# Kernel optimization log

Hardware: AMD Instinct MI355X
Metric: run time of the kernel (lower is better)

The kernel has to match this reference:

```python
import jax, jax.numpy as jnp
import numpy as np

B, S, L, T = 32, 512, 20, 16
E, H, D = 300, 128, 128
V = 50000
SEG = S // T


def _gru_dir(x, Wi, Wh, bi, bh, reverse):
    """One direction of torch-style GRU. x: (B,S,E). Returns (outs (B,S,H), h_final (B,H))."""
    xs = jnp.swapaxes(x, 0, 1)  # (S,B,E)
    h0 = jnp.zeros((x.shape[0], H), x.dtype)

    def step(h, x_t):
        gi = x_t @ Wi.T + bi          # (B,3H) gates order: r,z,n (torch)
        gh = h @ Wh.T + bh
        r = jax.nn.sigmoid(gi[:, :H] + gh[:, :H])
        z = jax.nn.sigmoid(gi[:, H:2 * H] + gh[:, H:2 * H])
        n = jnp.tanh(gi[:, 2 * H:] + r * gh[:, 2 * H:])
        h_new = (1.0 - z) * n + z * h
        return h_new, h_new

    hN, hs = jax.lax.scan(step, h0, xs, reverse=reverse)
    return jnp.swapaxes(hs, 0, 1), hN


def setup_inputs() -> dict:
    key = jax.random.key(0)
    ks = jax.random.split(key, 16)
    word_ids = jax.random.randint(ks[0], (B, S, L), 0, V, dtype=jnp.int32)
    # contiguous, full-coverage topic segments, 1-based boundaries (as in the torch code)
    starts = jnp.tile(jnp.arange(T, dtype=jnp.int32) * SEG + 1, (B, 1))
    ends = jnp.tile((jnp.arange(T, dtype=jnp.int32) + 1) * SEG, (B, 1))
    sent2topic = jnp.tile((jnp.arange(S, dtype=jnp.int32) // SEG), (B, 1))
    sc = 0.08
    return {
        "word_ids": word_ids, "starts": starts, "ends": ends, "sent2topic": sent2topic,
        "embed_table": jax.random.normal(ks[1], (V, E), jnp.float32) * 0.6,
        "Wi_f": jax.random.normal(ks[2], (3 * H, E), jnp.float32) * sc,
        "Wh_f": jax.random.normal(ks[3], (3 * H, H), jnp.float32) * sc,
        "bi_f": jax.random.normal(ks[4], (3 * H,), jnp.float32) * sc,
        "bh_f": jax.random.normal(ks[5], (3 * H,), jnp.float32) * sc,
        "Wi_b": jax.random.normal(ks[6], (3 * H, E), jnp.float32) * sc,
        "Wh_b": jax.random.normal(ks[7], (3 * H, H), jnp.float32) * sc,
        "bi_b": jax.random.normal(ks[8], (3 * H,), jnp.float32) * sc,
        "bh_b": jax.random.normal(ks[9], (3 * H,), jnp.float32) * sc,
        "W_att": jax.random.normal(ks[10], (4 * H, 4 * H), jnp.float32) * 0.05,
        "v_att": jax.random.normal(ks[11], (4 * H, 1), jnp.float32) * 0.05,
        "W1": jax.random.normal(ks[12], (D, 4 * H), jnp.float32) * 0.05,
        "b1": jax.random.normal(ks[13], (D,), jnp.float32) * 0.05,
        "W2": jax.random.normal(ks[14], (1, D), jnp.float32) * 0.05,
        "b2": jax.random.normal(ks[15], (1,), jnp.float32) * 0.05,
    }


def reference(word_ids, starts, ends, sent2topic, embed_table,
              Wi_f, Wh_f, bi_f, bh_f, Wi_b, Wh_b, bi_b, bh_b,
              W_att, v_att, W1, b1, W2, b2):
    # --- sent_encoder: mean of word embeddings per sentence ---
    sent = jnp.take(embed_table, word_ids, axis=0).mean(axis=2)  # (B,S,E)
    # --- doc_encoder: bidirectional GRU ---
    out_f, h_f = _gru_dir(sent, Wi_f, Wh_f, bi_f, bh_f, reverse=False)
    out_b, h_b = _gru_dir(sent, Wi_b, Wh_b, bi_b, bh_b, reverse=True)
    sent_rep = jnp.concatenate([out_f, out_b], axis=-1)          # (B,S,2H)
    # faithful to torch: hidden (2,B,H).view(B,2H)
    hidden = jnp.stack([h_f, h_b], axis=0)
    doc_rep = hidden.reshape(B, 2 * H)
    doc_rep = jnp.broadcast_to(doc_rep[None], (S, B, 2 * H)).swapaxes(0, 1)  # (B,S,2H)
    # --- topic_rep: boundary diffs (padded index i == 1-based sentence i) ---
    padded = jnp.pad(sent_rep, ((0, 0), (1, 1), (0, 0)))          # (B,S+2,2H)
    g = lambda idx: jnp.take_along_axis(padded, idx[:, :, None], axis=1)  # (B,T,2H)
    fwd_diff = g(ends)[..., :H] - g(starts - 1)[..., :H]
    bwd_diff = g(starts)[..., H:] - g(ends + 1)[..., H:]
    topic_mat = jnp.concatenate([fwd_diff, bwd_diff], axis=-1)   # (B,T,2H)
    topic_rep = jnp.take_along_axis(topic_mat, sent2topic[:, :, None], axis=1)  # (B,S,2H)
    # --- decoder ---
    cat_ds = jnp.concatenate([doc_rep, sent_rep], axis=-1)       # (B,S,4H)
    cat_ts = jnp.concatenate([topic_rep, sent_rep], axis=-1)
    doc_scores = jnp.tanh(cat_ds @ W_att) @ v_att                # (B,S,1)
    topic_scores = jnp.tanh(cat_ts @ W_att) @ v_att
    sum_scores = doc_scores + topic_scores
    doc_w = doc_scores / sum_scores
    topic_w = topic_scores / sum_scores
    context = doc_w * doc_rep + topic_w * topic_rep
    inp = jnp.concatenate([sent_rep, context], axis=-1)          # (B,S,4H)
    h = jax.nn.relu(inp @ W1.T + b1)                             # dropout=eval identity
    logits = (h @ W2.T + b2).squeeze(-1)                         # (B,S)
    return logits
```

## Files before the change

### kernel.cpp

```cpp
#include <hip/hip_runtime.h>


#define LDS_BARRIER() do {                                   \
    asm volatile("s_waitcnt lgkmcnt(0)" ::: "memory");       \
    __builtin_amdgcn_s_barrier();                            \
    asm volatile("" ::: "memory");                           \
  } while (0)

__global__ __launch_bounds__(256) void k_wcat(
    const float* __restrict__ wf, const float* __restrict__ wb,
    const float* __restrict__ bf, const float* __restrict__ bb,
    float* __restrict__ Wcat, float* __restrict__ bcat)
{
  const int idx = blockIdx.x * 256 + threadIdx.x;
  Wcat[idx] = wf[idx];
  Wcat[115200 + idx] = wb[idx];
  if (idx < 384) { bcat[idx] = bf[idx]; bcat[384 + idx] = bb[idx]; }
}

__global__ __launch_bounds__(128) void k_sent_mean(
    const int* __restrict__ wid, const float* __restrict__ emb,
    float* __restrict__ sent)
{
  const int bs = blockIdx.x;
  const int t = threadIdx.x;
  const int* w = wid + (size_t)bs * 20;
  if (t >= 75) return;
  float4 a = {0.f, 0.f, 0.f, 0.f};
  for (int l = 0; l < 20; ++l) {
    const float4 v = *(const float4*)(emb + (size_t)w[l] * 300 + t * 4);
    a.x += v.x; a.y += v.y; a.z += v.z; a.w += v.w;
  }
  const float inv = 1.0f / 20.0f;
  a.x *= inv; a.y *= inv; a.z *= inv; a.w *= inv;
  *(float4*)(sent + (size_t)bs * 300 + t * 4) = a;
}

template<bool BT, int ACT>
__global__ __launch_bounds__(256) void k_gemm(
    const int M, const int N, const int K,
    const float* __restrict__ A, const int lda,
    const float* __restrict__ Bm, const int ldb,
    float* __restrict__ C, const int ldc,
    const float* __restrict__ bias)
{
  (void)N;
  __shared__ float Ast[64][68];
  __shared__ float Bs[64][68];
  const int tid = threadIdx.x;
  const int m0 = blockIdx.x * 64;
  const int n0 = blockIdx.y * 64;
  const int tx = tid & 15;
  const int ty = tid >> 4;
  float acc[4][4] = {};

  for (int kc = 0; kc < K; kc += 64) {
    const int kb = (K - kc < 64) ? (K - kc) : 64;
    #pragma unroll
    for (int r = 0; r < 4; ++r) {
      const int m = r * 16 + ty;
      const int k4 = tx * 4;
      float4 v = make_float4(0.f, 0.f, 0.f, 0.f);
      if (m0 + m < M) {
        const float* ap = A + (size_t)(m0 + m) * lda + kc;
        if (k4 + 4 <= kb) {
          v = *(const float4*)(ap + k4);
        } else {
          float t0 = (k4 + 0 < kb) ? ap[k4 + 0] : 0.f;
          float t1 = (k4 + 1 < kb) ? ap[k4 + 1] : 0.f;
          float t2 = (k4 + 2 < kb) ? ap[k4 + 2] : 0.f;
          float t3 = (k4 + 3 < kb) ? ap[k4 + 3] : 0.f;
          v = make_float4(t0, t1, t2, t3);
        }
      }
      Ast[k4 + 0][m] = v.x;
      Ast[k4 + 1][m] = v.y;
      Ast[k4 + 2][m] = v.z;
      Ast[k4 + 3][m] = v.w;
    }
    if (BT) {
      #pragma unroll
      for (int r = 0; r < 4; ++r) {
        const int n = r * 16 + ty;
        const int k4 = tx * 4;
        float4 v = make_float4(0.f, 0.f, 0.f, 0.f);
        const float* bp = Bm + (size_t)(n0 + n) * ldb + kc;
        if (k4 + 4 <= kb) {
          v = *(const float4*)(bp + k4);
        } else {
          float t0 = (k4 + 0 < kb) ? bp[k4 + 0] : 0.f;
          float t1 = (k4 + 1 < kb) ? bp[k4 + 1] : 0.f;
          float t2 = (k4 + 2 < kb) ? bp[k4 + 2] : 0.f;
          float t3 = (k4 + 3 < kb) ? bp[k4 + 3] : 0.f;
          v = make_float4(t0, t1, t2, t3);
        }
        Bs[k4 + 0][n] = v.x;
        Bs[k4 + 1][n] = v.y;
        Bs[k4 + 2][n] = v.z;
        Bs[k4 + 3][n] = v.w;
      }
    } else {
      #pragma unroll
      for (int r = 0; r < 4; ++r) {
        const int kk = r * 16 + ty;
        const int n4 = tx * 4;
        float4 v = make_float4(0.f, 0.f, 0.f, 0.f);
        if (kk < kb) v = *(const float4*)(Bm + (size_t)(kc + kk) * ldb + n0 + n4);
        *(float4*)&Bs[kk][n4] = v;
      }
    }
    __syncthreads();
    #pragma unroll 4
    for (int kk = 0; kk < kb; ++kk) {
      const float4 av = *(const float4*)&Ast[kk][ty * 4];
      const float4 bv = *(const float4*)&Bs[kk][tx * 4];
      acc[0][0] = fmaf(av.x, bv.x, acc[0][0]);
      acc[0][1] = fmaf(av.x, bv.y, acc[0][1]);
      acc[0][2] = fmaf(av.x, bv.z, acc[0][2]);
      acc[0][3] = fmaf(av.x, bv.w, acc[0][3]);
      acc[1][0] = fmaf(av.y, bv.x, acc[1][0]);
      acc[1][1] = fmaf(av.y, bv.y, acc[1][1]);
      acc[1][2] = fmaf(av.y, bv.z, acc[1][2]);
      acc[1][3] = fmaf(av.y, bv.w, acc[1][3]);
      acc[2][0] = fmaf(av.z, bv.x, acc[2][0]);
      acc[2][1] = fmaf(av.z, bv.y, acc[2][1]);
      acc[2][2] = fmaf(av.z, bv.z, acc[2][2]);
      acc[2][3] = fmaf(av.z, bv.w, acc[2][3]);
      acc[3][0] = fmaf(av.w, bv.x, acc[3][0]);
      acc[3][1] = fmaf(av.w, bv.y, acc[3][1]);
      acc[3][2] = fmaf(av.w, bv.z, acc[3][2]);
      acc[3][3] = fmaf(av.w, bv.w, acc[3][3]);
    }
    __syncthreads();
  }

  float bv4[4] = {0.f, 0.f, 0.f, 0.f};
  if (bias != nullptr) {
    #pragma unroll
    for (int j = 0; j < 4; ++j) bv4[j] = bias[n0 + tx * 4 + j];
  }
  #pragma unroll
  for (int i = 0; i < 4; ++i) {
    const int m = m0 + ty * 4 + i;
    if (m < M) {
      float4 o;
      o.x = acc[i][0] + bv4[0];
      o.y = acc[i][1] + bv4[1];
      o.z = acc[i][2] + bv4[2];
      o.w = acc[i][3] + bv4[3];
      if (ACT == 1) {
        o.x = fmaxf(o.x, 0.f); o.y = fmaxf(o.y, 0.f);
        o.z = fmaxf(o.z, 0.f); o.w = fmaxf(o.w, 0.f);
      }
      *(float4*)&C[(size_t)m * ldc + n0 + tx * 4] = o;
    }
  }
}

__global__ __launch_bounds__(512, 2) void k_gru(
    const float* __restrict__ gi_fb,
    const float* __restrict__ Wh_f, const float* __restrict__ Wh_b,
    const float* __restrict__ bh_f, const float* __restrict__ bh_b,
    float* __restrict__ srep, float* __restrict__ hfin)
{
  const int dir = blockIdx.x & 1;
  const int b = blockIdx.x >> 1;
  const float* gi = gi_fb + (size_t)b * 512 * 768 + dir * 384;
  const float* Wh = dir ? Wh_b : Wh_f;
  const float* bh = dir ? bh_b : bh_f;

  const int tid = threadIdx.x;
  const int wv = tid >> 6;
  const int ln = tid & 63;
  const int kq = wv & 3;
  const int rg = wv >> 2;
  const int r0 = rg * 192 + ln;

  __shared__ __align__(16) float hlds[128];
  __shared__ float partl[4 * 384];
  __shared__ __align__(16) float gis[2][32 * 384];

  float4 w0[8], w1[8], w2[8];
  {
    const float* p = Wh + (size_t)r0 * 128 + kq * 32;
    #pragma unroll
    for (int kk = 0; kk < 8; ++kk) w0[kk] = *(const float4*)(p + kk * 4);
    p += 64 * 128;
    #pragma unroll
    for (int kk = 0; kk < 8; ++kk) w1[kk] = *(const float4*)(p + kk * 4);
    p += 64 * 128;
    #pragma unroll
    for (int kk = 0; kk < 8; ++kk) w2[kk] = *(const float4*)(p + kk * 4);
  }
  const float bh0 = (kq == 0) ? bh[r0] : 0.f;
  const float bh1 = (kq == 0) ? bh[r0 + 64] : 0.f;
  const float bh2 = (kq == 0) ? bh[r0 + 128] : 0.f;

  {
    const int lo0 = dir ? 480 : 0;
    const float4* g4 = (const float4*)(gi + (size_t)lo0 * 768);
    float4* l4 = (float4*)gis[0];
    #pragma unroll
    for (int j = 0; j < 6; ++j) {
      const int f = j * 512 + tid;
      const int row = f / 96;
      const int col = f - row * 96;
      l4[f] = g4[row * 192 + col];
    }
  }
  float hreg = 0.f;
  if (tid < 128) hlds[tid] = 0.f;
  LDS_BARRIER();

  const float4* h4q = (const float4*)hlds + kq * 8;
  float4 stg[6];

  for (int c = 0; c < 16; ++c) {
    const int buf = c & 1;
    const int lo = dir ? (480 - 32 * c) : (32 * c);
    if (c < 15) {
      const int lon = dir ? (480 - 32 * (c + 1)) : (32 * (c + 1));
      const float4* g4 = (const float4*)(gi + (size_t)lon * 768);
      #pragma unroll
      for (int j = 0; j < 6; ++j) {
        const int f = j * 512 + tid;
        const int row = f / 96;
        const int col = f - row * 96;
        stg[j] = g4[row * 192 + col];
      }
    }

    for (int i = 0; i < 32; ++i) {
      const int sloc = dir ? (31 - i) : i;
      const int seq = lo + sloc;

      float4 A0 = {0.f, 0.f, 0.f, 0.f};
      float4 A1 = {0.f, 0.f, 0.f, 0.f};
      float4 A2 = {0.f, 0.f, 0.f, 0.f};
      #pragma unroll
      for (int kk = 0; kk < 8; ++kk) {
        const float4 hv = h4q[kk];
        A0.x = fmaf(w0[kk].x, hv.x, A0.x);
        A0.y = fmaf(w0[kk].y, hv.y, A0.y);
        A0.z = fmaf(w0[kk].z, hv.z, A0.z);
        A0.w = fmaf(w0[kk].w, hv.w, A0.w);
        A1.x = fmaf(w1[kk].x, hv.x, A1.x);
        A1.y = fmaf(w1[kk].y, hv.y, A1.y);
        A1.z = fmaf(w1[kk].z, hv.z, A1.z);
        A1.w = fmaf(w1[kk].w, hv.w, A1.w);
        A2.x = fmaf(w2[kk].x, hv.x, A2.x);
        A2.y = fmaf(w2[kk].y, hv.y, A2.y);
        A2.z = fmaf(w2[kk].z, hv.z, A2.z);
        A2.w = fmaf(w2[kk].w, hv.w, A2.w);
      }
      partl[kq * 384 + r0]       = (A0.x + A0.y) + (A0.z + A0.w) + bh0;
      partl[kq * 384 + r0 + 64]  = (A1.x + A1.y) + (A1.z + A1.w) + bh1;
      partl[kq * 384 + r0 + 128] = (A2.x + A2.y) + (A2.z + A2.w) + bh2;
      LDS_BARRIER();

      if (tid < 128) {
        const float* grow = &gis[buf][sloc * 384];
        const float ghr = (partl[tid]       + partl[384 + tid])
                        + (partl[768 + tid] + partl[1152 + tid]);
        const float ghz = (partl[tid + 128]        + partl[384 + tid + 128])
                        + (partl[768 + tid + 128]  + partl[1152 + tid + 128]);
        const float ghn = (partl[tid + 256]        + partl[384 + tid + 256])
                        + (partl[768 + tid + 256]  + partl[1152 + tid + 256]);
        const float gir = grow[tid];
        const float giz = grow[tid + 128];
        const float gin = grow[tid + 256];
        const float r = __fdividef(1.f, 1.f + __expf(-(gir + ghr)));
        const float z = __fdividef(1.f, 1.f + __expf(-(giz + ghz)));
        float an = gin + r * ghn;
        an = fminf(fmaxf(an, -15.f), 15.f);
        const float t = __expf(2.f * an);
        const float n = __fdividef(t - 1.f, t + 1.f);
        hreg = (1.f - z) * n + z * hreg;
        hlds[tid] = hreg;
        srep[((size_t)(b * 512 + seq)) * 256 + dir * 128 + tid] = hreg;
      }
      LDS_BARRIER();
    }

    if (c < 15) {
      float4* l4 = (float4*)gis[buf ^ 1];
      #pragma unroll
      for (int j = 0; j < 6; ++j) l4[j * 512 + tid] = stg[j];
      LDS_BARRIER();
    }
  }
  if (tid < 128) hfin[(size_t)dir * 4096 + (size_t)b * 128 + tid] = hreg;
}

__global__ __launch_bounds__(256) void k_topic(
    const int* __restrict__ starts, const int* __restrict__ ends,
    const float* __restrict__ srep, float* __restrict__ tmat)
{
  const int bt = blockIdx.x;
  const int b = bt >> 4;
  const int st = starts[bt], en = ends[bt];
  const int j = threadIdx.x;
  float v;
  if (j < 128) {
    const float a = (en >= 1 && en <= 512) ? srep[((size_t)(b * 512 + en - 1)) * 256 + j] : 0.f;
    const float c = (st - 1 >= 1 && st - 1 <= 512) ? srep[((size_t)(b * 512 + st - 2)) * 256 + j] : 0.f;
    v = a - c;
  } else {
    const float a = (st >= 1 && st <= 512) ? srep[((size_t)(b * 512 + st - 1)) * 256 + j] : 0.f;
    const float c = (en + 1 >= 1 && en + 1 <= 512) ? srep[((size_t)(b * 512 + en)) * 256 + j] : 0.f;
    v = a - c;
  }
  tmat[(size_t)bt * 256 + j] = v;
}

__global__ __launch_bounds__(256) void k_scores(
    const float* spart, const float* __restrict__ docp, const float* __restrict__ topp,
    const float* __restrict__ v_att, const float* __restrict__ srep,
    const float* __restrict__ docrep, const float* __restrict__ tmat,
    const int* __restrict__ s2t, float* inp)
{
  const int bs = blockIdx.x;
  const int b = bs >> 9;
  const int tid = threadIdx.x;
  const int tp = s2t[bs];
  const float* sp = spart + (size_t)bs * 512;
  const float* dp = docp + (size_t)b * 512;
  const float* tq = topp + ((size_t)(b * 16 + tp)) * 512;
  float ds = 0.f, ts = 0.f;
  #pragma unroll
  for (int r = 0; r < 2; ++r) {
    const int o = tid + r * 256;
    const float s0 = sp[o], v = v_att[o];
    ds += tanhf(s0 + dp[o]) * v;
    ts += tanhf(s0 + tq[o]) * v;
  }
  #pragma unroll
  for (int off = 32; off; off >>= 1) {
    ds += __shfl_down(ds, off);
    ts += __shfl_down(ts, off);
  }
  __shared__ float rds[4], rts[4], wsh[2];
  const int wv = tid >> 6, ln = tid & 63;
  if (ln == 0) { rds[wv] = ds; rts[wv] = ts; }
  __syncthreads();
  if (tid == 0) {
    const float D = rds[0] + rds[1] + rds[2] + rds[3];
    const float T = rts[0] + rts[1] + rts[2] + rts[3];
    const float sum = D + T;
    wsh[0] = D / sum;
    wsh[1] = T / sum;
  }
  __syncthreads();
  const float dw = wsh[0], tw = wsh[1];
  const float sr = srep[(size_t)bs * 256 + tid];
  const float ctx = dw * docrep[(size_t)b * 256 + tid]
                  + tw * tmat[((size_t)(b * 16 + tp)) * 256 + tid];
  float* op = inp + (size_t)bs * 512;
  op[tid] = sr;
  op[256 + tid] = ctx;
}

__global__ __launch_bounds__(64) void k_logits(
    const float* __restrict__ hbuf, const float* __restrict__ W2,
    const float* __restrict__ b2, float* __restrict__ out)
{
  const int bs = blockIdx.x;
  const int ln = threadIdx.x;
  const float* h = hbuf + (size_t)bs * 128;
  float a = fmaf(h[ln], W2[ln], h[ln + 64] * W2[ln + 64]);
  #pragma unroll
  for (int off = 32; off; off >>= 1) a += __shfl_down(a, off);
  if (ln == 0) out[bs] = a + b2[0];
}

extern "C" void kernel_launch(void* const* d_in, const int* in_sizes, int n_in,
                              void* d_out, int out_size, void* d_ws, size_t ws_size,
                              hipStream_t stream)
{
  (void)in_sizes; (void)n_in; (void)out_size;

  const int*   word_ids = (const int*)d_in[0];
  const int*   starts   = (const int*)d_in[1];
  const int*   ends     = (const int*)d_in[2];
  const int*   s2t      = (const int*)d_in[3];
  const float* emb      = (const float*)d_in[4];
  const float* Wi_f     = (const float*)d_in[5];
  const float* Wh_f     = (const float*)d_in[6];
  const float* bi_f     = (const float*)d_in[7];
  const float* bh_f     = (const float*)d_in[8];
  const float* Wi_b     = (const float*)d_in[9];
  const float* Wh_b     = (const float*)d_in[10];
  const float* bi_b     = (const float*)d_in[11];
  const float* bh_b     = (const float*)d_in[12];
  const float* W_att    = (const float*)d_in[13];
  const float* v_att    = (const float*)d_in[14];
  const float* W1       = (const float*)d_in[15];
  const float* b1       = (const float*)d_in[16];
  const float* W2       = (const float*)d_in[17];
  const float* b2       = (const float*)d_in[18];
  float* out = (float*)d_out;

  char* ws = (char*)d_ws;
  if (ws_size < 88440832u) return;
  float* sent  = (float*)(ws + 0);
  float* gi_fb = (float*)(ws + 19660800);
  float* srep  = (float*)(ws + 69992448);
  float* hfin  = (float*)(ws + 86769664);
  float* tmat  = (float*)(ws + 86802432);
  float* docp  = (float*)(ws + 87326720);
  float* topp  = (float*)(ws + 87392256);
  float* spart = (float*)(ws + 19660800);
  float* hbuf  = (float*)(ws + 0);
  float* Wcat  = (float*)(ws + 69992448);
  float* bcat  = (float*)(ws + 70914048);

  k_sent_mean<<<16384, 128, 0, stream>>>(word_ids, emb, sent);
  k_wcat<<<450, 256, 0, stream>>>(Wi_f, Wi_b, bi_f, bi_b, Wcat, bcat);
  k_gemm<true, 0><<<dim3(256, 12), 256, 0, stream>>>(16384, 768, 300, sent, 300, Wcat, 300, gi_fb, 768, bcat);
  k_gru<<<64, 512, 0, stream>>>(gi_fb, Wh_f, Wh_b, bh_f, bh_b, srep, hfin);
  k_topic<<<512, 256, 0, stream>>>(starts, ends, srep, tmat);
  k_gemm<false, 0><<<dim3(256, 8), 256, 0, stream>>>(16384, 512, 256, srep, 256, W_att + 256 * 512, 512, spart, 512, nullptr);
  k_gemm<false, 0><<<dim3(1, 8),   256, 0, stream>>>(32,    512, 256, hfin, 256, W_att,            512, docp,  512, nullptr);
  k_gemm<false, 0><<<dim3(8, 8),   256, 0, stream>>>(512,   512, 256, tmat, 256, W_att,            512, topp,  512, nullptr);
  k_scores<<<16384, 256, 0, stream>>>(spart, docp, topp, v_att, srep, hfin, tmat, s2t, spart);
  k_gemm<true, 1><<<dim3(256, 2), 256, 0, stream>>>(16384, 128, 512, spart, 512, W1, 512, hbuf, 128, b1);
  k_logits<<<16384, 64, 0, stream>>>(hbuf, W2, b2, out);
}
```

Before: 710.8 us.

## Enlarge GEMM tiles to 128x128 and keep GRU recurrent weights in AGPRs

```diff
diff --git a/kernel.cpp b/kernel.cpp
--- a/kernel.cpp
+++ b/kernel.cpp
@@ -6,6 +6,11 @@
     __builtin_amdgcn_s_barrier();                            \
     asm volatile("" ::: "memory");                           \
   } while (0)
+
+#define AGPR_WRITE(dst, src) \
+  asm volatile("v_accvgpr_write_b32 %0, %1" : "=a"(dst) : "v"(src))
+#define AGPR_READ(dst, src) \
+  asm volatile("v_accvgpr_read_b32 %0, %1" : "=v"(dst) : "a"(src))
 
 __global__ __launch_bounds__(256) void k_wcat(
     const float* __restrict__ wf, const float* __restrict__ wb,
@@ -45,32 +50,32 @@
     const float* __restrict__ bias)
 {
   (void)N;
-  __shared__ float Ast[64][68];
-  __shared__ float Bs[64][68];
+  __shared__ float Ast[32][132];
+  __shared__ float Bs[32][132];
   const int tid = threadIdx.x;
-  const int m0 = blockIdx.x * 64;
-  const int n0 = blockIdx.y * 64;
+  const int m0 = blockIdx.x * 128;
+  const int n0 = blockIdx.y * 128;
   const int tx = tid & 15;
   const int ty = tid >> 4;
-  float acc[4][4] = {};
-
-  for (int kc = 0; kc < K; kc += 64) {
-    const int kb = (K - kc < 64) ? (K - kc) : 64;
-    #pragma unroll
-    for (int r = 0; r < 4; ++r) {
-      const int m = r * 16 + ty;
-      const int k4 = tx * 4;
+  float acc[2][4][2][4] = {};
+
+  for (int kc = 0; kc < K; kc += 32) {
+    const int kb = (K - kc < 32) ? (K - kc) : 32;
+    #pragma unroll
+    for (int j = 0; j < 4; ++j) {
+      const int f = j * 256 + tid;
+      const int m = f >> 3;
+      const int k4 = (f & 7) * 4;
       float4 v = make_float4(0.f, 0.f, 0.f, 0.f);
       if (m0 + m < M) {
         const float* ap = A + (size_t)(m0 + m) * lda + kc;
         if (k4 + 4 <= kb) {
           v = *(const float4*)(ap + k4);
         } else {
-          float t0 = (k4 + 0 < kb) ? ap[k4 + 0] : 0.f;
-          float t1 = (k4 + 1 < kb) ? ap[k4 + 1] : 0.f;
-          float t2 = (k4 + 2 < kb) ? ap[k4 + 2] : 0.f;
-          float t3 = (k4 + 3 < kb) ? ap[k4 + 3] : 0.f;
-          v = make_float4(t0, t1, t2, t3);
+          if (k4 + 0 < kb) v.x = ap[k4 + 0];
+          if (k4 + 1 < kb) v.y = ap[k4 + 1];
+          if (k4 + 2 < kb) v.z = ap[k4 + 2];
+          if (k4 + 3 < kb) v.w = ap[k4 + 3];
         }
       }
       Ast[k4 + 0][m] = v.x;
@@ -80,19 +85,19 @@
     }
     if (BT) {
       #pragma unroll
-      for (int r = 0; r < 4; ++r) {
-        const int n = r * 16 + ty;
-        const int k4 = tx * 4;
+      for (int j = 0; j < 4; ++j) {
+        const int f = j * 256 + tid;
+        const int n = f >> 3;
+        const int k4 = (f & 7) * 4;
         float4 v = make_float4(0.f, 0.f, 0.f, 0.f);
         const float* bp = Bm + (size_t)(n0 + n) * ldb + kc;
         if (k4 + 4 <= kb) {
           v = *(const float4*)(bp + k4);
         } else {
-          float t0 = (k4 + 0 < kb) ? bp[k4 + 0] : 0.f;
-          float t1 = (k4 + 1 < kb) ? bp[k4 + 1] : 0.f;
-          float t2 = (k4 + 2 < kb) ? bp[k4 + 2] : 0.f;
-          float t3 = (k4 + 3 < kb) ? bp[k4 + 3] : 0.f;
-          v = make_float4(t0, t1, t2, t3);
+          if (k4 + 0 < kb) v.x = bp[k4 + 0];
+          if (k4 + 1 < kb) v.y = bp[k4 + 1];
+          if (k4 + 2 < kb) v.z = bp[k4 + 2];
+          if (k4 + 3 < kb) v.w = bp[k4 + 3];
         }
         Bs[k4 + 0][n] = v.x;
         Bs[k4 + 1][n] = v.y;
@@ -101,60 +106,66 @@
       }
     } else {
       #pragma unroll
-      for (int r = 0; r < 4; ++r) {
-        const int kk = r * 16 + ty;
-        const int n4 = tx * 4;
+      for (int j = 0; j < 4; ++j) {
+        const int f = j * 256 + tid;
+        const int kk = f >> 5;
+        const int n4 = (f & 31) * 4;
         float4 v = make_float4(0.f, 0.f, 0.f, 0.f);
         if (kk < kb) v = *(const float4*)(Bm + (size_t)(kc + kk) * ldb + n0 + n4);
         *(float4*)&Bs[kk][n4] = v;
       }
     }
     __syncthreads();
-    #pragma unroll 4
+    #pragma unroll 2
     for (int kk = 0; kk < kb; ++kk) {
-      const float4 av = *(const float4*)&Ast[kk][ty * 4];
-      const float4 bv = *(const float4*)&Bs[kk][tx * 4];
-      acc[0][0] = fmaf(av.x, bv.x, acc[0][0]);
-      acc[0][1] = fmaf(av.x, bv.y, acc[0][1]);
-      acc[0][2] = fmaf(av.x, bv.z, acc[0][2]);
-      acc[0][3] = fmaf(av.x, bv.w, acc[0][3]);
-      acc[1][0] = fmaf(av.y, bv.x, acc[1][0]);
-      acc[1][1] = fmaf(av.y, bv.y, acc[1][1]);
-      acc[1][2] = fmaf(av.y, bv.z, acc[1][2]);
-      acc[1][3] = fmaf(av.y, bv.w, acc[1][3]);
-      acc[2][0] = fmaf(av.z, bv.x, acc[2][0]);
-      acc[2][1] = fmaf(av.z, bv.y, acc[2][1]);
-      acc[2][2] = fmaf(av.z, bv.z, acc[2][2]);
-      acc[2][3] = fmaf(av.z, bv.w, acc[2][3]);
-      acc[3][0] = fmaf(av.w, bv.x, acc[3][0]);
-      acc[3][1] = fmaf(av.w, bv.y, acc[3][1]);
-      acc[3][2] = fmaf(av.w, bv.z, acc[3][2]);
-      acc[3][3] = fmaf(av.w, bv.w, acc[3][3]);
+      const float4 a0 = *(const float4*)&Ast[kk][ty * 4];
+      const float4 a1 = *(const float4*)&Ast[kk][64 + ty * 4];
+      const float4 b0 = *(const float4*)&Bs[kk][tx * 4];
+      const float4 b1 = *(const float4*)&Bs[kk][64 + tx * 4];
+      const float av[2][4] = {{a0.x, a0.y, a0.z, a0.w}, {a1.x, a1.y, a1.z, a1.w}};
+      const float bv[2][4] = {{b0.x, b0.y, b0.z, b0.w}, {b1.x, b1.y, b1.z, b1.w}};
+      #pragma unroll
+      for (int ih = 0; ih < 2; ++ih)
+        #pragma unroll
+        for (int i = 0; i < 4; ++i)
+          #pragma unroll
+          for (int jh = 0; jh < 2; ++jh)
+            #pragma unroll
+            for (int j = 0; j < 4; ++j)
+              acc[ih][i][jh][j] = fmaf(av[ih][i], bv[jh][j], acc[ih][i][jh][j]);
     }
     __syncthreads();
   }
 
-  float bv4[4] = {0.f, 0.f, 0.f, 0.f};
+  float bv4[2][4] = {};
   if (bias != nullptr) {
     #pragma unroll
-    for (int j = 0; j < 4; ++j) bv4[j] = bias[n0 + tx * 4 + j];
+    for (int jh = 0; jh < 2; ++jh)
+      #pragma unroll
+      for (int j = 0; j < 4; ++j)
+        bv4[jh][j] = bias[n0 + jh * 64 + tx * 4 + j];
   }
   #pragma unroll
-  for (int i = 0; i < 4; ++i) {
-    const int m = m0 + ty * 4 + i;
-    if (m < M) {
-      float4 o;
-      o.x = acc[i][0] + bv4[0];
-      o.y = acc[i][1] + bv4[1];
-      o.z = acc[i][2] + bv4[2];
-      o.w = acc[i][3] + bv4[3];
-      if (ACT == 1) {
-        o.x = fmaxf(o.x, 0.f); o.y = fmaxf(o.y, 0.f);
-        o.z = fmaxf(o.z, 0.f); o.w = fmaxf(o.w, 0.f);
-      }
-      *(float4*)&C[(size_t)m * ldc + n0 + tx * 4] = o;
-    }
-  }
+  for (int ih = 0; ih < 2; ++ih)
+    #pragma unroll
+    for (int i = 0; i < 4; ++i) {
+      const int m = m0 + ih * 64 + ty * 4 + i;
+      if (m < M) {
+        #pragma unroll
+        for (int jh = 0; jh < 2; ++jh) {
+          float4 o;
+          o.x = acc[ih][i][jh][0] + bv4[jh][0];
+          o.y = acc[ih][i][jh][1] + bv4[jh][1];
+          o.z = acc[ih][i][jh][2] + bv4[jh][2];
+          o.w = acc[ih][i][jh][3] + bv4[jh][3];
+          if (ACT == 1) {
+            o.x = fmaxf(o.x, 0.f); o.y = fmaxf(o.y, 0.f);
+            o.z = fmaxf(o.z, 0.f); o.w = fmaxf(o.w, 0.f);
+          }
+          *(float4*)&C[(size_t)m * ldc + n0 + jh * 64 + tx * 4] = o;
+        }
+      }
+    }
 }
 
 __global__ __launch_bounds__(512, 2) void k_gru(
@@ -180,17 +191,29 @@
   __shared__ float partl[4 * 384];
   __shared__ __align__(16) float gis[2][32 * 384];
 
-  float4 w0[8], w1[8], w2[8];
+  float aw0[32], aw1[32], aw2[32];
   {
     const float* p = Wh + (size_t)r0 * 128 + kq * 32;
     #pragma unroll
-    for (int kk = 0; kk < 8; ++kk) w0[kk] = *(const float4*)(p + kk * 4);
+    for (int k = 0; k < 32; k += 4) {
+      const float4 v = *(const float4*)(p + k);
+      AGPR_WRITE(aw0[k + 0], v.x); AGPR_WRITE(aw0[k + 1], v.y);
+      AGPR_WRITE(aw0[k + 2], v.z); AGPR_WRITE(aw0[k + 3], v.w);
+    }
     p += 64 * 128;
     #pragma unroll
-    for (int kk = 0; kk < 8; ++kk) w1[kk] = *(const float4*)(p + kk * 4);
+    for (int k = 0; k < 32; k += 4) {
+      const float4 v = *(const float4*)(p + k);
+      AGPR_WRITE(aw1[k + 0], v.x); AGPR_WRITE(aw1[k + 1], v.y);
+      AGPR_WRITE(aw1[k + 2], v.z); AGPR_WRITE(aw1[k + 3], v.w);
+    }
     p += 64 * 128;
     #pragma unroll
-    for (int kk = 0; kk < 8; ++kk) w2[kk] = *(const float4*)(p + kk * 4);
+    for (int k = 0; k < 32; k += 4) {
+      const float4 v = *(const float4*)(p + k);
+      AGPR_WRITE(aw2[k + 0], v.x); AGPR_WRITE(aw2[k + 1], v.y);
+      AGPR_WRITE(aw2[k + 2], v.z); AGPR_WRITE(aw2[k + 3], v.w);
+    }
   }
   const float bh0 = (kq == 0) ? bh[r0] : 0.f;
   const float bh1 = (kq == 0) ? bh[r0 + 64] : 0.f;
@@ -240,18 +263,19 @@
       #pragma unroll
       for (int kk = 0; kk < 8; ++kk) {
         const float4 hv = h4q[kk];
-        A0.x = fmaf(w0[kk].x, hv.x, A0.x);
-        A0.y = fmaf(w0[kk].y, hv.y, A0.y);
-        A0.z = fmaf(w0[kk].z, hv.z, A0.z);
-        A0.w = fmaf(w0[kk].w, hv.w, A0.w);
-        A1.x = fmaf(w1[kk].x, hv.x, A1.x);
-        A1.y = fmaf(w1[kk].y, hv.y, A1.y);
-        A1.z = fmaf(w1[kk].z, hv.z, A1.z);
-        A1.w = fmaf(w1[kk].w, hv.w, A1.w);
-        A2.x = fmaf(w2[kk].x, hv.x, A2.x);
-        A2.y = fmaf(w2[kk].y, hv.y, A2.y);
-        A2.z = fmaf(w2[kk].z, hv.z, A2.z);
-        A2.w = fmaf(w2[kk].w, hv.w, A2.w);
+        float w;
+        AGPR_READ(w, aw0[kk * 4 + 0]); A0.x = fmaf(w, hv.x, A0.x);
+        AGPR_READ(w, aw0[kk * 4 + 1]); A0.y = fmaf(w, hv.y, A0.y);
+        AGPR_READ(w, aw0[kk * 4 + 2]); A0.z = fmaf(w, hv.z, A0.z);
+        AGPR_READ(w, aw0[kk * 4 + 3]); A0.w = fmaf(w, hv.w, A0.w);
+        AGPR_READ(w, aw1[kk * 4 + 0]); A1.x = fmaf(w, hv.x, A1.x);
+        AGPR_READ(w, aw1[kk * 4 + 1]); A1.y = fmaf(w, hv.y, A1.y);
+        AGPR_READ(w, aw1[kk * 4 + 2]); A1.z = fmaf(w, hv.z, A1.z);
+        AGPR_READ(w, aw1[kk * 4 + 3]); A1.w = fmaf(w, hv.w, A1.w);
+        AGPR_READ(w, aw2[kk * 4 + 0]); A2.x = fmaf(w, hv.x, A2.x);
+        AGPR_READ(w, aw2[kk * 4 + 1]); A2.y = fmaf(w, hv.y, A2.y);
+        AGPR_READ(w, aw2[kk * 4 + 2]); A2.z = fmaf(w, hv.z, A2.z);
+        AGPR_READ(w, aw2[kk * 4 + 3]); A2.w = fmaf(w, hv.w, A2.w);
       }
       partl[kq * 384 + r0]       = (A0.x + A0.y) + (A0.z + A0.w) + bh0;
       partl[kq * 384 + r0 + 64]  = (A1.x + A1.y) + (A1.z + A1.w) + bh1;
@@ -416,13 +440,13 @@
 
   k_sent_mean<<<16384, 128, 0, stream>>>(word_ids, emb, sent);
   k_wcat<<<450, 256, 0, stream>>>(Wi_f, Wi_b, bi_f, bi_b, Wcat, bcat);
-  k_gemm<true, 0><<<dim3(256, 12), 256, 0, stream>>>(16384, 768, 300, sent, 300, Wcat, 300, gi_fb, 768, bcat);
+  k_gemm<true, 0><<<dim3(128, 6), 256, 0, stream>>>(16384, 768, 300, sent, 300, Wcat, 300, gi_fb, 768, bcat);
   k_gru<<<64, 512, 0, stream>>>(gi_fb, Wh_f, Wh_b, bh_f, bh_b, srep, hfin);
   k_topic<<<512, 256, 0, stream>>>(starts, ends, srep, tmat);
-  k_gemm<false, 0><<<dim3(256, 8), 256, 0, stream>>>(16384, 512, 256, srep, 256, W_att + 256 * 512, 512, spart, 512, nullptr);
-  k_gemm<false, 0><<<dim3(1, 8),   256, 0, stream>>>(32,    512, 256, hfin, 256, W_att,            512, docp,  512, nullptr);
-  k_gemm<false, 0><<<dim3(8, 8),   256, 0, stream>>>(512,   512, 256, tmat, 256, W_att,            512, topp,  512, nullptr);
+  k_gemm<false, 0><<<dim3(128, 4), 256, 0, stream>>>(16384, 512, 256, srep, 256, W_att + 256 * 512, 512, spart, 512, nullptr);
+  k_gemm<false, 0><<<dim3(1, 4),   256, 0, stream>>>(32,    512, 256, hfin, 256, W_att,            512, docp,  512, nullptr);
+  k_gemm<false, 0><<<dim3(4, 4),   256, 0, stream>>>(512,   512, 256, tmat, 256, W_att,            512, topp,  512, nullptr);
   k_scores<<<16384, 256, 0, stream>>>(spart, docp, topp, v_att, srep, hfin, tmat, s2t, spart);
-  k_gemm<true, 1><<<dim3(256, 2), 256, 0, stream>>>(16384, 128, 512, spart, 512, W1, 512, hbuf, 128, b1);
+  k_gemm<true, 1><<<dim3(128, 1), 256, 0, stream>>>(16384, 128, 512, spart, 512, W1, 512, hbuf, 128, b1);
   k_logits<<<16384, 64, 0, stream>>>(hbuf, W2, b2, out);
 }
```

Measured after the change: 965.9 us. 35.9% more time.

## Split GRU recurrent weights between LDS and registers, halve gi chunk size

Applied to the files above, without the earlier changes.

```diff
diff --git a/kernel.cpp b/kernel.cpp
--- a/kernel.cpp
+++ b/kernel.cpp
@@ -176,13 +176,25 @@
   const int rg = wv >> 2;
   const int r0 = rg * 192 + ln;
 
+  __shared__ float4 wlds4[384 * 16];
   __shared__ __align__(16) float hlds[128];
   __shared__ float partl[4 * 384];
-  __shared__ __align__(16) float gis[2][32 * 384];
+  __shared__ __align__(16) float gis[2][16 * 384];
+
+  {
+    const float4* Wh4 = (const float4*)Wh;
+    #pragma unroll
+    for (int j = 0; j < 12; ++j) {
+      const int idx = j * 512 + tid;
+      const int row = idx >> 4;
+      const int lslot = idx & 15;
+      wlds4[(row << 4) + (lslot ^ (row & 7))] = Wh4[row * 32 + lslot];
+    }
+  }
 
   float4 w0[8], w1[8], w2[8];
-  {
-    const float* p = Wh + (size_t)r0 * 128 + kq * 32;
+  if (kq >= 2) {
+    const float* p = Wh + (size_t)r0 * 128 + 64 + (kq - 2) * 32;
     #pragma unroll
     for (int kk = 0; kk < 8; ++kk) w0[kk] = *(const float4*)(p + kk * 4);
     p += 64 * 128;
@@ -197,11 +209,11 @@
   const float bh2 = (kq == 0) ? bh[r0 + 128] : 0.f;
 
   {
-    const int lo0 = dir ? 480 : 0;
+    const int lo0 = dir ? 496 : 0;
     const float4* g4 = (const float4*)(gi + (size_t)lo0 * 768);
     float4* l4 = (float4*)gis[0];
     #pragma unroll
-    for (int j = 0; j < 6; ++j) {
+    for (int j = 0; j < 3; ++j) {
       const int f = j * 512 + tid;
       const int row = f / 96;
       const int col = f - row * 96;
@@ -213,16 +225,20 @@
   LDS_BARRIER();
 
   const float4* h4q = (const float4*)hlds + kq * 8;
-  float4 stg[6];
-
-  for (int c = 0; c < 16; ++c) {
+  const int sw = ln & 7;
+  const float4* wl0 = wlds4 + (r0 << 4) + kq * 8;
+  const float4* wl1 = wl0 + (64 << 4);
+  const float4* wl2 = wl0 + (128 << 4);
+  float4 stg[3];
+
+  for (int c = 0; c < 32; ++c) {
     const int buf = c & 1;
-    const int lo = dir ? (480 - 32 * c) : (32 * c);
-    if (c < 15) {
-      const int lon = dir ? (480 - 32 * (c + 1)) : (32 * (c + 1));
+    const int lo = dir ? (496 - 16 * c) : (16 * c);
+    if (c < 31) {
+      const int lon = dir ? (496 - 16 * (c + 1)) : (16 * (c + 1));
       const float4* g4 = (const float4*)(gi + (size_t)lon * 768);
       #pragma unroll
-      for (int j = 0; j < 6; ++j) {
+      for (int j = 0; j < 3; ++j) {
         const int f = j * 512 + tid;
         const int row = f / 96;
         const int col = f - row * 96;
@@ -230,28 +246,50 @@
       }
     }
 
-    for (int i = 0; i < 32; ++i) {
-      const int sloc = dir ? (31 - i) : i;
+    for (int i = 0; i < 16; ++i) {
+      const int sloc = dir ? (15 - i) : i;
       const int seq = lo + sloc;
 
       float4 A0 = {0.f, 0.f, 0.f, 0.f};
       float4 A1 = {0.f, 0.f, 0.f, 0.f};
       float4 A2 = {0.f, 0.f, 0.f, 0.f};
-      #pragma unroll
-      for (int kk = 0; kk < 8; ++kk) {
-        const float4 hv = h4q[kk];
-        A0.x = fmaf(w0[kk].x, hv.x, A0.x);
-        A0.y = fmaf(w0[kk].y, hv.y, A0.y);
-        A0.z = fmaf(w0[kk].z, hv.z, A0.z);
-        A0.w = fmaf(w0[kk].w, hv.w, A0.w);
-        A1.x = fmaf(w1[kk].x, hv.x, A1.x);
-        A1.y = fmaf(w1[kk].y, hv.y, A1.y);
-        A1.z = fmaf(w1[kk].z, hv.z, A1.z);
-        A1.w = fmaf(w1[kk].w, hv.w, A1.w);
-        A2.x = fmaf(w2[kk].x, hv.x, A2.x);
-        A2.y = fmaf(w2[kk].y, hv.y, A2.y);
-        A2.z = fmaf(w2[kk].z, hv.z, A2.z);
-        A2.w = fmaf(w2[kk].w, hv.w, A2.w);
+      if (kq < 2) {
+        #pragma unroll
+        for (int jj = 0; jj < 8; ++jj) {
+          const float4 hv = h4q[jj];
+          const float4 q0 = wl0[jj ^ sw];
+          const float4 q1 = wl1[jj ^ sw];
+          const float4 q2 = wl2[jj ^ sw];
+          A0.x = fmaf(q0.x, hv.x, A0.x);
+          A0.y = fmaf(q0.y, hv.y, A0.y);
+          A0.z = fmaf(q0.z, hv.z, A0.z);
+          A0.w = fmaf(q0.w, hv.w, A0.w);
+          A1.x = fmaf(q1.x, hv.x, A1.x);
+          A1.y = fmaf(q1.y, hv.y, A1.y);
+          A1.z = fmaf(q1.z, hv.z, A1.z);
+          A1.w = fmaf(q1.w, hv.w, A1.w);
+          A2.x = fmaf(q2.x, hv.x, A2.x);
+          A2.y = fmaf(q2.y, hv.y, A2.y);
+          A2.z = fmaf(q2.z, hv.z, A2.z);
+          A2.w = fmaf(q2.w, hv.w, A2.w);
+        }
+      } else {
+        #pragma unroll
+        for (int kk = 0; kk < 8; ++kk) {
+          const float4 hv = h4q[kk];
+          A0.x = fmaf(w0[kk].x, hv.x, A0.x);
+          A0.y = fmaf(w0[kk].y, hv.y, A0.y);
+          A0.z = fmaf(w0[kk].z, hv.z, A0.z);
+          A0.w = fmaf(w0[kk].w, hv.w, A0.w);
+          A1.x = fmaf(w1[kk].x, hv.x, A1.x);
+          A1.y = fmaf(w1[kk].y, hv.y, A1.y);
+          A1.z = fmaf(w1[kk].z, hv.z, A1.z);
+          A1.w = fmaf(w1[kk].w, hv.w, A1.w);
+          A2.x = fmaf(w2[kk].x, hv.x, A2.x);
+          A2.y = fmaf(w2[kk].y, hv.y, A2.y);
+          A2.z = fmaf(w2[kk].z, hv.z, A2.z);
+          A2.w = fmaf(w2[kk].w, hv.w, A2.w);
+        }
       }
       partl[kq * 384 + r0]       = (A0.x + A0.y) + (A0.z + A0.w) + bh0;
       partl[kq * 384 + r0 + 64]  = (A1.x + A1.y) + (A1.z + A1.w) + bh1;
@@ -282,10 +320,10 @@
       LDS_BARRIER();
     }
 
-    if (c < 15) {
+    if (c < 31) {
       float4* l4 = (float4*)gis[buf ^ 1];
       #pragma unroll
-      for (int j = 0; j < 6; ++j) l4[j * 512 + tid] = stg[j];
+      for (int j = 0; j < 3; ++j) l4[j * 512 + tid] = stg[j];
       LDS_BARRIER();
     }
   }
```

New measurement: 918.9 us. 29.3% more time.
